# Kernel tuning notes

Hardware: AMD Instinct MI355X
Metric: run time of the kernel (lower is better)

Reference implementation:

```python
import jax, jax.numpy as jnp
import numpy as np

B, T, D, H, F = 2, 128, 256, 8, 64
C = H * F          # channels = 512
TEMB = 512         # time_embed_dim


def setup_inputs() -> dict:
    key = jax.random.key(0)
    ks = jax.random.split(key, 9)
    qk = jax.random.normal(ks[0], (B, D, H, T, F), jnp.float32)
    # integer-valued relative distances in [-(T-1), T-1], stored as float
    pairwise_distances = jax.random.randint(ks[1], (B, T, T), -(T - 1), T).astype(jnp.float32)
    temb = jax.random.normal(ks[2], (B, T, TEMB), jnp.float32)
    # linear layer params (note: original zero-inits w_out/b_out; we use random
    # values so the kernel correctness test is non-trivial)
    w_dist = jax.random.normal(ks[3], (C, 3), jnp.float32) / np.sqrt(3.0)
    b_dist = jax.random.normal(ks[4], (C,), jnp.float32) * 0.02
    w_time = jax.random.normal(ks[5], (C, TEMB), jnp.float32) / np.sqrt(TEMB)
    b_time = jax.random.normal(ks[6], (C,), jnp.float32) * 0.02
    w_out = jax.random.normal(ks[7], (C, C), jnp.float32) / np.sqrt(C)
    b_out = jax.random.normal(ks[8], (C,), jnp.float32) * 0.02
    return {"qk": qk, "pairwise_distances": pairwise_distances, "temb": temb,
            "w_dist": w_dist, "b_dist": b_dist, "w_time": w_time, "b_time": b_time,
            "w_out": w_out, "b_out": b_out}


def _rpe_net(pd, temb, w_dist, b_dist, w_time, b_time, w_out, b_out):
    # distance features: [B,T,T,3]
    dist_embs = jnp.stack([
        jnp.log1p(jnp.maximum(pd, 0.0)),
        jnp.log1p(jnp.maximum(-pd, 0.0)),
        (pd == 0).astype(pd.dtype),
    ], axis=-1)
    # [B,T,1,C] + [B,T,T,C]
    temb_emb = jnp.einsum('btk,ck->btc', temb, w_time) + b_time
    emb = temb_emb[:, :, None, :] + jnp.einsum('btsk,ck->btsc', dist_embs, w_dist) + b_dist
    r = jnp.einsum('btsc,oc->btso', jax.nn.silu(emb), w_out) + b_out
    return r.reshape(B, T, T, H, F)  # [B,T,S,H,F]


def reference(qk, pairwise_distances, temb, w_dist, b_dist, w_time, b_time, w_out, b_out):
    R = _rpe_net(pairwise_distances, temb, w_dist, b_dist, w_time, b_time, w_out, b_out)
    # mode == 'qk'
    return jnp.einsum('bdhtf,btshf->bdhts', qk, R)
```

## Files before the change

### kernel.cpp

```cpp
#include <hip/hip_runtime.h>
#include <hip/hip_bf16.h>
#include <math.h>

typedef __attribute__((ext_vector_type(8))) short short8;
typedef __attribute__((ext_vector_type(4))) float f32x4;

#define B_    2
#define T_    128
#define D_    256
#define H_    8
#define F_    64
#define C_    512
#define TEMB_ 512

static __device__ __forceinline__ unsigned short f2bf(float f) {
  __hip_bfloat16 h = __float2bfloat16(f);
  return reinterpret_cast<unsigned short&>(h);
}
static __device__ __forceinline__ unsigned int pk2(float a, float b) {
  return (unsigned int)f2bf(a) | ((unsigned int)f2bf(b) << 16);
}

__global__ __launch_bounds__(256) void k_pre(
    const float* __restrict__ temb, const float* __restrict__ w_time,
    const float* __restrict__ b_time, const float* __restrict__ b_dist,
    const float* __restrict__ w_out, const float* __restrict__ w_dist,
    float* __restrict__ base, short* __restrict__ wsw, float* __restrict__ wdT)
{
  const int tid = threadIdx.x;
  if (blockIdx.x >= 64) {
    int gid = (blockIdx.x - 64) * 256 + tid;
    for (int s = gid; s < 32768; s += 16384) {
      int oi = s >> 10, rem = s & 1023, kjg = rem >> 6, l = rem & 63;
      int o = oi * 16 + (l & 15), c = kjg * 32 + (l >> 4) * 8;
      const float* src = w_out + (size_t)o * C_ + c;
      float4 a = *reinterpret_cast<const float4*>(src);
      float4 b = *reinterpret_cast<const float4*>(src + 4);
      uint4 v; v.x = pk2(a.x, a.y); v.y = pk2(a.z, a.w);
      v.z = pk2(b.x, b.y); v.w = pk2(b.z, b.w);
      *reinterpret_cast<uint4*>(wsw + (size_t)s * 8) = v;
    }
    if (gid < C_) {
      wdT[0 * C_ + gid] = w_dist[gid * 3 + 0];
      wdT[1 * C_ + gid] = w_dist[gid * 3 + 1];
      wdT[2 * C_ + gid] = w_dist[gid * 3 + 2];
    }
    return;
  }
  __shared__ float tt[32][64];
  __shared__ float wt[64][65];
  const int bt0 = (blockIdx.x & 7) * 32;
  const int c0  = (blockIdx.x >> 3) * 64;
  const int cl  = tid & 63;
  const int g   = tid >> 6;
  float acc[8] = {0.f,0.f,0.f,0.f,0.f,0.f,0.f,0.f};

  for (int k0 = 0; k0 < TEMB_; k0 += 64) {
#pragma unroll
    for (int i = 0; i < 8; ++i) {
      int idx = tid + i * 256; int r = idx >> 6, k = idx & 63;
      tt[r][k] = temb[(size_t)(bt0 + r) * TEMB_ + k0 + k];
    }
#pragma unroll
    for (int i = 0; i < 16; ++i) {
      int idx = tid + i * 256; int r = idx >> 6, k = idx & 63;
      wt[r][k] = w_time[(size_t)(c0 + r) * TEMB_ + k0 + k];
    }
    __syncthreads();
#pragma unroll
    for (int k = 0; k < 64; ++k) {
      float w = wt[cl][k];
#pragma unroll
      for (int j = 0; j < 8; ++j) acc[j] += tt[g + 4 * j][k] * w;
    }
    __syncthreads();
  }
  float bb = b_time[c0 + cl] + b_dist[c0 + cl];
#pragma unroll
  for (int j = 0; j < 8; ++j)
    base[(size_t)(bt0 + g + 4 * j) * C_ + c0 + cl] = acc[j] + bb;
}

__global__ __launch_bounds__(512, 4) void k_rpe(
    const float* __restrict__ pd, const float* __restrict__ base,
    const float* __restrict__ wdT, const short* __restrict__ wsw,
    const float* __restrict__ b_out, unsigned short* __restrict__ Rg)
{
  __shared__ __align__(16) short At[8192];
  __shared__ float df[3][T_];

  const int bx   = blockIdx.x;
  const int bt   = bx >> 1;
  const int half = bx & 1;
  const int b    = bt >> 7;
  const int t    = bt & 127;
  const int tid  = threadIdx.x;
  const int lane = tid & 63;
  const int wave = tid >> 6;
  const int lanem = lane & 15;
  const int laneg = lane >> 4;

  if (tid < T_) {
    float p = pd[((size_t)b * T_ + t) * T_ + tid];
    df[0][tid] = log1pf(fmaxf(p, 0.f));
    df[1][tid] = log1pf(fmaxf(-p, 0.f));
    df[2][tid] = (p == 0.f) ? 1.f : 0.f;
  }

  const int wm = wave >> 2;
  const int wn = wave & 3;
  const int s_low = tid & 15;
  const int cg    = (tid >> 4) & 7;
  const int si_b  = (tid >> 7) * 2;
  const int kjA   = cg >> 2;
  const int cgl   = cg & 3;
  const int laneslotA = s_low + 16 * cgl;
  const float* baserow = base + (size_t)bt * C_;

  f32x4 acc[4][4];
#pragma unroll
  for (int mi = 0; mi < 4; ++mi)
#pragma unroll
    for (int ni = 0; ni < 4; ++ni) acc[mi][ni] = (f32x4){0.f, 0.f, 0.f, 0.f};

  for (int kt = 0; kt < 8; ++kt) {
    __syncthreads();
    short8 b0[4], b1[4];
#pragma unroll
    for (int ni = 0; ni < 4; ++ni) {
      int oi = half * 16 + wn * 4 + ni;
      b0[ni] = *reinterpret_cast<const short8*>(
          wsw + ((size_t)(oi * 16 + kt * 2 + 0) * 64 + lane) * 8);
    }
    {
      const int cglob = kt * 64 + cg * 8;
      float4 bs0 = *reinterpret_cast<const float4*>(baserow + cglob);
      float4 bs1 = *reinterpret_cast<const float4*>(baserow + cglob + 4);
      float4 wa0 = *reinterpret_cast<const float4*>(wdT + cglob);
      float4 wa1 = *reinterpret_cast<const float4*>(wdT + cglob + 4);
      float4 wb0 = *reinterpret_cast<const float4*>(wdT + C_ + cglob);
      float4 wb1 = *reinterpret_cast<const float4*>(wdT + C_ + cglob + 4);
      float4 wc0 = *reinterpret_cast<const float4*>(wdT + 2 * C_ + cglob);
      float4 wc1 = *reinterpret_cast<const float4*>(wdT + 2 * C_ + cglob + 4);
#pragma unroll
      for (int q = 0; q < 2; ++q) {
        int si = si_b + q;
        int s  = si * 16 + s_low;
        float d0 = df[0][s], d1 = df[1][s], d2 = df[2][s];
        uint4 v;
        {
          float x0 = bs0.x + d0 * wa0.x + d1 * wb0.x + d2 * wc0.x;
          float x1 = bs0.y + d0 * wa0.y + d1 * wb0.y + d2 * wc0.y;
          float x2 = bs0.z + d0 * wa0.z + d1 * wb0.z + d2 * wc0.z;
          float x3 = bs0.w + d0 * wa0.w + d1 * wb0.w + d2 * wc0.w;
          x0 = x0 / (1.f + __expf(-x0)); x1 = x1 / (1.f + __expf(-x1));
          x2 = x2 / (1.f + __expf(-x2)); x3 = x3 / (1.f + __expf(-x3));
          v.x = pk2(x0, x1); v.y = pk2(x2, x3);
        }
        {
          float x0 = bs1.x + d0 * wa1.x + d1 * wb1.x + d2 * wc1.x;
          float x1 = bs1.y + d0 * wa1.y + d1 * wb1.y + d2 * wc1.y;
          float x2 = bs1.z + d0 * wa1.z + d1 * wb1.z + d2 * wc1.z;
          float x3 = bs1.w + d0 * wa1.w + d1 * wb1.w + d2 * wc1.w;
          x0 = x0 / (1.f + __expf(-x0)); x1 = x1 / (1.f + __expf(-x1));
          x2 = x2 / (1.f + __expf(-x2)); x3 = x3 / (1.f + __expf(-x3));
          v.z = pk2(x0, x1); v.w = pk2(x2, x3);
        }
        *reinterpret_cast<uint4*>(&At[((si * 2 + kjA) * 64 + laneslotA) * 8]) = v;
      }
    }
#pragma unroll
    for (int ni = 0; ni < 4; ++ni) {
      int oi = half * 16 + wn * 4 + ni;
      b1[ni] = *reinterpret_cast<const short8*>(
          wsw + ((size_t)(oi * 16 + kt * 2 + 1) * 64 + lane) * 8);
    }
    __syncthreads();
    {
      short8 a[4];
#pragma unroll
      for (int mi = 0; mi < 4; ++mi)
        a[mi] = *reinterpret_cast<const short8*>(
            &At[(((wm * 4 + mi) * 2 + 0) * 64 + lane) * 8]);
#pragma unroll
      for (int ni = 0; ni < 4; ++ni)
#pragma unroll
        for (int mi = 0; mi < 4; ++mi)
          acc[mi][ni] = __builtin_amdgcn_mfma_f32_16x16x32_bf16(
              b0[ni], a[mi], acc[mi][ni], 0, 0, 0);
#pragma unroll
      for (int mi = 0; mi < 4; ++mi)
        a[mi] = *reinterpret_cast<const short8*>(
            &At[(((wm * 4 + mi) * 2 + 1) * 64 + lane) * 8]);
#pragma unroll
      for (int ni = 0; ni < 4; ++ni)
#pragma unroll
        for (int mi = 0; mi < 4; ++mi)
          acc[mi][ni] = __builtin_amdgcn_mfma_f32_16x16x32_bf16(
              b1[ni], a[mi], acc[mi][ni], 0, 0, 0);
    }
  }

  unsigned short* Rbt = Rg + (size_t)bt * T_ * C_;
#pragma unroll
  for (int ni = 0; ni < 4; ++ni) {
    const int o0 = half * 256 + wn * 64 + ni * 16 + laneg * 4;
    const float4 bo4 = *reinterpret_cast<const float4*>(b_out + o0);
#pragma unroll
    for (int mi = 0; mi < 4; ++mi) {
      const int s = wm * 64 + mi * 16 + lanem;
      uint2 v;
      v.x = pk2(acc[mi][ni][0] + bo4.x, acc[mi][ni][1] + bo4.y);
      v.y = pk2(acc[mi][ni][2] + bo4.z, acc[mi][ni][3] + bo4.w);
      *reinterpret_cast<uint2*>(Rbt + (size_t)s * C_ + o0) = v;
    }
  }
}

__global__ __launch_bounds__(256, 4) void k_qkr(
    const float* __restrict__ qk, const unsigned short* __restrict__ Rg,
    float* __restrict__ out)
{
  __shared__ __align__(16) float stage[4][2048];

  const int bx = blockIdx.x;
  const int h  = bx & 7;
  const int bt = bx >> 3;
  const int b  = bt >> 7;
  const int t  = bt & 127;
  const int tid  = threadIdx.x;
  const int lane = tid & 63;
  const int wave = tid >> 6;
  const int lanem = lane & 15;
  const int laneg = lane >> 4;
  const int d0w = wave * 64;

  const size_t HTF = (size_t)H_ * T_ * F_;
  const size_t HTT = (size_t)H_ * T_ * T_;
  const float* qkb = qk + (size_t)b * D_ * HTF + (size_t)h * T_ * F_ + (size_t)t * F_;
  float* outb = out + (size_t)b * D_ * HTT + (size_t)h * T_ * T_ + (size_t)t * T_;
  const unsigned short* Rb = Rg + (size_t)bt * T_ * C_ + h * F_;

  float4 buf[4];
  {
    const float* src = qkb + (size_t)(d0w + lanem) * HTF + laneg * 8;
    buf[0] = *reinterpret_cast<const float4*>(src);
    buf[1] = *reinterpret_cast<const float4*>(src + 4);
    buf[2] = *reinterpret_cast<const float4*>(src + 32);
    buf[3] = *reinterpret_cast<const float4*>(src + 36);
  }

  short8 brf[2][8];
#pragma unroll
  for (int kj = 0; kj < 2; ++kj)
#pragma unroll
    for (int ni = 0; ni < 8; ++ni)
      brf[kj][ni] = *reinterpret_cast<const short8*>(
          Rb + (size_t)(ni * 16 + lanem) * C_ + kj * 32 + laneg * 8);

  char* stO = (char*)stage[wave];
  const int xw = lanem << 4;
  const int l5 = lane >> 5;
  const int sb = (lane & 31) * 16;

  for (int cc = 0; cc < 4; ++cc) {
    const int dbase = d0w + cc * 16;
    short8 qb0, qb1;
    {
      union { uint4 u; short8 s; } cv;
      cv.u.x = pk2(buf[0].x, buf[0].y); cv.u.y = pk2(buf[0].z, buf[0].w);
      cv.u.z = pk2(buf[1].x, buf[1].y); cv.u.w = pk2(buf[1].z, buf[1].w);
      qb0 = cv.s;
      cv.u.x = pk2(buf[2].x, buf[2].y); cv.u.y = pk2(buf[2].z, buf[2].w);
      cv.u.z = pk2(buf[3].x, buf[3].y); cv.u.w = pk2(buf[3].z, buf[3].w);
      qb1 = cv.s;
    }
    if (cc < 3) {
      const float* src = qkb + (size_t)(dbase + 16 + lanem) * HTF + laneg * 8;
      buf[0] = *reinterpret_cast<const float4*>(src);
      buf[1] = *reinterpret_cast<const float4*>(src + 4);
      buf[2] = *reinterpret_cast<const float4*>(src + 32);
      buf[3] = *reinterpret_cast<const float4*>(src + 36);
    }
    f32x4 ac[8];
#pragma unroll
    for (int ni = 0; ni < 8; ++ni) ac[ni] = (f32x4){0.f, 0.f, 0.f, 0.f};
#pragma unroll
    for (int ni = 0; ni < 8; ++ni)
      ac[ni] = __builtin_amdgcn_mfma_f32_16x16x32_bf16(brf[0][ni], qb0, ac[ni], 0, 0, 0);
#pragma unroll
    for (int ni = 0; ni < 8; ++ni)
      ac[ni] = __builtin_amdgcn_mfma_f32_16x16x32_bf16(brf[1][ni], qb1, ac[ni], 0, 0, 0);
#pragma unroll
    for (int ni = 0; ni < 8; ++ni)
      *reinterpret_cast<f32x4*>(
          stO + lanem * 512 + ((ni * 64 + laneg * 16) ^ xw)) = ac[ni];
#pragma unroll
    for (int i = 0; i < 8; ++i) {
      int r = i * 2 + l5;
      float4 v = *reinterpret_cast<const float4*>(
          stO + r * 512 + (sb ^ (r << 4)));
      *reinterpret_cast<float4*>(
          outb + (size_t)(dbase + r) * HTT + (lane & 31) * 4) = v;
    }
  }
}

extern "C" void kernel_launch(void* const* d_in, const int* in_sizes, int n_in,
                              void* d_out, int out_size, void* d_ws, size_t ws_size,
                              hipStream_t stream) {
  const float* qk     = (const float*)d_in[0];
  const float* pd     = (const float*)d_in[1];
  const float* temb   = (const float*)d_in[2];
  const float* w_dist = (const float*)d_in[3];
  const float* b_dist = (const float*)d_in[4];
  const float* w_time = (const float*)d_in[5];
  const float* b_time = (const float*)d_in[6];
  const float* w_out  = (const float*)d_in[7];
  const float* b_out  = (const float*)d_in[8];
  float* out = (float*)d_out;

  char* ws = (char*)d_ws;
  float* base          = (float*)(ws);
  float* wdT           = (float*)(ws + 524288);
  short* wsw           = (short*)(ws + 532480);
  unsigned short* Rg   = (unsigned short*)(ws + 1056768);

  hipLaunchKernelGGL(k_pre, dim3(128), dim3(256), 0, stream,
                     temb, w_time, b_time, b_dist, w_out, w_dist,
                     base, wsw, wdT);
  hipLaunchKernelGGL(k_rpe, dim3(2 * B_ * T_), dim3(512), 0, stream,
                     pd, base, wdT, wsw, b_out, Rg);
  hipLaunchKernelGGL(k_qkr, dim3(B_ * T_ * H_), dim3(256), 0, stream,
                     qk, Rg, out);
}
```

Baseline: 203.1 us.

## Remap qk·R kernel grid over d-groups and t-quarters, drop LDS staging

Each k_qkr block now covers a group of 16 d values and a quarter of t for a single (b,h), where before it covered one (b,t,h) across all d. Each wave loops over 8 t values, reloading the R tile and qk rows for every t. Because each t maps to a contiguous output row, the LDS transpose stage is removed and results are written straight to global memory as float4. The cost is that R is re-read from global or L2 by every d-group (16x reuse across blocks instead of within a block), and the output stores become 64-byte pieces per row rather than 512-byte coalesced rows.

```diff
diff --git a/kernel.cpp b/kernel.cpp
--- a/kernel.cpp
+++ b/kernel.cpp
@@ -221,88 +221,69 @@
     const float* __restrict__ qk, const unsigned short* __restrict__ Rg,
     float* __restrict__ out)
 {
-  __shared__ __align__(16) float stage[4][2048];
-
   const int bx = blockIdx.x;
-  const int h  = bx & 7;
-  const int bt = bx >> 3;
-  const int b  = bt >> 7;
-  const int t  = bt & 127;
+  const int g  = bx & 63;
+  const int dg = bx >> 6;
+  const int b  = g >> 5;
+  const int h  = (g >> 2) & 7;
+  const int tq = g & 3;
   const int tid  = threadIdx.x;
   const int lane = tid & 63;
   const int wave = tid >> 6;
   const int lanem = lane & 15;
   const int laneg = lane >> 4;
-  const int d0w = wave * 64;
 
   const size_t HTF = (size_t)H_ * T_ * F_;
   const size_t HTT = (size_t)H_ * T_ * T_;
-  const float* qkb = qk + (size_t)b * D_ * HTF + (size_t)h * T_ * F_ + (size_t)t * F_;
-  float* outb = out + (size_t)b * D_ * HTT + (size_t)h * T_ * T_ + (size_t)t * T_;
-  const unsigned short* Rb = Rg + (size_t)bt * T_ * C_ + h * F_;
-
-  float4 buf[4];
-  {
-    const float* src = qkb + (size_t)(d0w + lanem) * HTF + laneg * 8;
-    buf[0] = *reinterpret_cast<const float4*>(src);
-    buf[1] = *reinterpret_cast<const float4*>(src + 4);
-    buf[2] = *reinterpret_cast<const float4*>(src + 32);
-    buf[3] = *reinterpret_cast<const float4*>(src + 36);
-  }
-
-  short8 brf[2][8];
-#pragma unroll
-  for (int kj = 0; kj < 2; ++kj)
-#pragma unroll
-    for (int ni = 0; ni < 8; ++ni)
-      brf[kj][ni] = *reinterpret_cast<const short8*>(
-          Rb + (size_t)(ni * 16 + lanem) * C_ + kj * 32 + laneg * 8);
-
-  char* stO = (char*)stage[wave];
-  const int xw = lanem << 4;
-  const int l5 = lane >> 5;
-  const int sb = (lane & 31) * 16;
-
-  for (int cc = 0; cc < 4; ++cc) {
-    const int dbase = d0w + cc * 16;
+  const int d = dg * 16 + lanem;
+
+  const float* qkrow = qk + (size_t)b * D_ * HTF + (size_t)d * HTF
+                          + (size_t)h * T_ * F_ + laneg * 8;
+  float* outrow = out + (size_t)(b * D_ + d) * HTT + (size_t)h * T_ * T_;
+  const unsigned short* Rbase = Rg + (size_t)b * T_ * T_ * C_
+                                   + (size_t)lanem * C_ + h * F_ + laneg * 8;
+
+  const int t0 = tq * 32 + wave * 8;
+#pragma unroll
+  for (int ti = 0; ti < 8; ++ti) {
+    const int t = t0 + ti;
+    const float* qs = qkrow + (size_t)t * F_;
+    float4 q0 = *reinterpret_cast<const float4*>(qs);
+    float4 q1 = *reinterpret_cast<const float4*>(qs + 4);
+    float4 q2 = *reinterpret_cast<const float4*>(qs + 32);
+    float4 q3 = *reinterpret_cast<const float4*>(qs + 36);
+    const unsigned short* rs = Rbase + (size_t)t * T_ * C_;
+    short8 av[2][8];
+#pragma unroll
+    for (int kj = 0; kj < 2; ++kj)
+#pragma unroll
+      for (int ni = 0; ni < 8; ++ni)
+        av[kj][ni] = *reinterpret_cast<const short8*>(
+            rs + (size_t)ni * 16 * C_ + kj * 32);
     short8 qb0, qb1;
     {
       union { uint4 u; short8 s; } cv;
-      cv.u.x = pk2(buf[0].x, buf[0].y); cv.u.y = pk2(buf[0].z, buf[0].w);
-      cv.u.z = pk2(buf[1].x, buf[1].y); cv.u.w = pk2(buf[1].z, buf[1].w);
+      cv.u.x = pk2(q0.x, q0.y); cv.u.y = pk2(q0.z, q0.w);
+      cv.u.z = pk2(q1.x, q1.y); cv.u.w = pk2(q1.z, q1.w);
       qb0 = cv.s;
-      cv.u.x = pk2(buf[2].x, buf[2].y); cv.u.y = pk2(buf[2].z, buf[2].w);
-      cv.u.z = pk2(buf[3].x, buf[3].y); cv.u.w = pk2(buf[3].z, buf[3].w);
+      cv.u.x = pk2(q2.x, q2.y); cv.u.y = pk2(q2.z, q2.w);
+      cv.u.z = pk2(q3.x, q3.y); cv.u.w = pk2(q3.z, q3.w);
       qb1 = cv.s;
     }
-    if (cc < 3) {
-      const float* src = qkb + (size_t)(dbase + 16 + lanem) * HTF + laneg * 8;
-      buf[0] = *reinterpret_cast<const float4*>(src);
-      buf[1] = *reinterpret_cast<const float4*>(src + 4);
-      buf[2] = *reinterpret_cast<const float4*>(src + 32);
-      buf[3] = *reinterpret_cast<const float4*>(src + 36);
-    }
     f32x4 ac[8];
 #pragma unroll
     for (int ni = 0; ni < 8; ++ni) ac[ni] = (f32x4){0.f, 0.f, 0.f, 0.f};
 #pragma unroll
     for (int ni = 0; ni < 8; ++ni)
-      ac[ni] = __builtin_amdgcn_mfma_f32_16x16x32_bf16(brf[0][ni], qb0, ac[ni], 0, 0, 0);
+      ac[ni] = __builtin_amdgcn_mfma_f32_16x16x32_bf16(av[0][ni], qb0, ac[ni], 0, 0, 0);
 #pragma unroll
     for (int ni = 0; ni < 8; ++ni)
-      ac[ni] = __builtin_amdgcn_mfma_f32_16x16x32_bf16(brf[1][ni], qb1, ac[ni], 0, 0, 0);
+      ac[ni] = __builtin_amdgcn_mfma_f32_16x16x32_bf16(av[1][ni], qb1, ac[ni], 0, 0, 0);
+    float* os = outrow + (size_t)t * T_ + laneg * 4;
 #pragma unroll
     for (int ni = 0; ni < 8; ++ni)
-      *reinterpret_cast<f32x4*>(
-          stO + lanem * 512 + ((ni * 64 + laneg * 16) ^ xw)) = ac[ni];
-#pragma unroll
-    for (int i = 0; i < 8; ++i) {
-      int r = i * 2 + l5;
-      float4 v = *reinterpret_cast<const float4*>(
-          stO + r * 512 + (sb ^ (r << 4)));
-      *reinterpret_cast<float4*>(
-          outb + (size_t)(dbase + r) * HTT + (lane & 31) * 4) = v;
-    }
+      *reinterpret_cast<float4*>(os + ni * 16) =
+          (float4){ac[ni][0], ac[ni][1], ac[ni][2], ac[ni][3]};
   }
 }
 
@@ -331,6 +312,6 @@
                      base, wsw, wdT);
   hipLaunchKernelGGL(k_rpe, dim3(2 * B_ * T_), dim3(512), 0, stream,
                      pd, base, wdT, wsw, b_out, Rg);
-  hipLaunchKernelGGL(k_qkr, dim3(B_ * T_ * H_), dim3(256), 0, stream,
+  hipLaunchKernelGGL(k_qkr, dim3(1024), dim3(256), 0, stream,
                      qk, Rg, out);
 }
```

New measurement: 281.1 us. 1.38x slower.

## Stage qk tiles via async global-to-LDS DMA and store outputs directly

Applied to the files above, without the earlier changes.

Replaces register prefetch of qk rows with global_load_lds DMA into double-buffered, XOR-swizzled per-wave LDS buffers, using explicit vmcnt waits to overlap loads with MFMA work. The output transpose through LDS is dropped, and MFMA results are written straight to global as float4 per lane. This is meant to cut register pressure and LDS round-trips, but the direct stores use 16-byte segments scattered across rows, so they are less coalesced. The hand-counted vmcnt values are fragile if the compiler reorders memory operations.

```diff
diff --git a/kernel.cpp b/kernel.cpp
--- a/kernel.cpp
+++ b/kernel.cpp
@@ -12,6 +12,8 @@
 #define F_    64
 #define C_    512
 #define TEMB_ 512
+#define HTF_  65536
+#define HTT_  131072
 
 static __device__ __forceinline__ unsigned short f2bf(float f) {
   __hip_bfloat16 h = __float2bfloat16(f);
@@ -19,6 +21,12 @@
 }
 static __device__ __forceinline__ unsigned int pk2(float a, float b) {
   return (unsigned int)f2bf(a) | ((unsigned int)f2bf(b) << 16);
+}
+
+static __device__ __forceinline__ void dma16(const float* g, float* l) {
+  __builtin_amdgcn_global_load_lds(
+      (const __attribute__((address_space(1))) unsigned int*)g,
+      (__attribute__((address_space(3))) unsigned int*)l, 16, 0, 0);
 }
 
 __global__ __launch_bounds__(256) void k_pre(
@@ -221,7 +229,7 @@
     const float* __restrict__ qk, const unsigned short* __restrict__ Rg,
     float* __restrict__ out)
 {
-  __shared__ __align__(16) float stage[4][2048];
+  __shared__ __align__(16) float st[4][2][1024];
 
   const int bx = blockIdx.x;
   const int h  = bx & 7;
@@ -233,22 +241,10 @@
   const int wave = tid >> 6;
   const int lanem = lane & 15;
   const int laneg = lane >> 4;
-  const int d0w = wave * 64;
-
-  const size_t HTF = (size_t)H_ * T_ * F_;
-  const size_t HTT = (size_t)H_ * T_ * T_;
-  const float* qkb = qk + (size_t)b * D_ * HTF + (size_t)h * T_ * F_ + (size_t)t * F_;
-  float* outb = out + (size_t)b * D_ * HTT + (size_t)h * T_ * T_ + (size_t)t * T_;
+
+  const float* qkb = qk + (size_t)b * D_ * HTF_ + (size_t)h * T_ * F_ + (size_t)t * F_;
+  float* outb = out + (size_t)b * D_ * HTT_ + (size_t)h * T_ * T_ + (size_t)t * T_;
   const unsigned short* Rb = Rg + (size_t)bt * T_ * C_ + h * F_;
-
-  float4 buf[4];
-  {
-    const float* src = qkb + (size_t)(d0w + lanem) * HTF + laneg * 8;
-    buf[0] = *reinterpret_cast<const float4*>(src);
-    buf[1] = *reinterpret_cast<const float4*>(src + 4);
-    buf[2] = *reinterpret_cast<const float4*>(src + 32);
-    buf[3] = *reinterpret_cast<const float4*>(src + 36);
-  }
 
   short8 brf[2][8];
 #pragma unroll
@@ -258,29 +254,54 @@
       brf[kj][ni] = *reinterpret_cast<const short8*>(
           Rb + (size_t)(ni * 16 + lanem) * C_ + kj * 32 + laneg * 8);
 
-  char* stO = (char*)stage[wave];
-  const int xw = lanem << 4;
-  const int l5 = lane >> 5;
-  const int sb = (lane & 31) * 16;
-
-  for (int cc = 0; cc < 4; ++cc) {
-    const int dbase = d0w + cc * 16;
+  float* buf0 = &st[wave][0][0];
+  float* buf1 = &st[wave][1][0];
+  auto STAGE = [&](float* buf, int c) {
+#pragma unroll
+    for (int j = 0; j < 4; ++j) {
+      const int dl = j * 4 + laneg;
+      const int g  = lanem ^ ((dl & 7) << 1);
+      const float* src = qkb + (size_t)(c * 16 + dl) * HTF_ + g * 4;
+      dma16(src, buf + j * 256);
+    }
+  };
+
+  const int c0 = wave * 4;
+  STAGE(buf0, c0 + 0);
+  STAGE(buf1, c0 + 1);
+  __builtin_amdgcn_sched_barrier(0);
+
+#pragma unroll
+  for (int i = 0; i < 4; ++i) {
+    const int c = c0 + i;
+    float* cur = (i & 1) ? buf1 : buf0;
+    if (i == 0)      asm volatile("s_waitcnt vmcnt(4)"  ::: "memory");
+    else if (i == 1) asm volatile("s_waitcnt vmcnt(12)" ::: "memory");
+    else if (i == 2) asm volatile("s_waitcnt vmcnt(20)" ::: "memory");
+    else             asm volatile("s_waitcnt vmcnt(16)" ::: "memory");
+    __builtin_amdgcn_sched_barrier(0);
+
+    const int key = (lanem & 7) << 1;
+    const int bd  = lanem * 64;
+    const int g0  = (2 * laneg) ^ key;
+    const int g1  = (8 + 2 * laneg) ^ key;
+    float4 f0 = *reinterpret_cast<const float4*>(cur + bd + g0 * 4);
+    float4 f1 = *reinterpret_cast<const float4*>(cur + bd + g0 * 4 + 4);
+    float4 f2 = *reinterpret_cast<const float4*>(cur + bd + g1 * 4);
+    float4 f3 = *reinterpret_cast<const float4*>(cur + bd + g1 * 4 + 4);
+    asm volatile("s_waitcnt lgkmcnt(0)" ::: "memory");
+    __builtin_amdgcn_sched_barrier(0);
+    if (i < 2) STAGE(cur, c + 2);
+
     short8 qb0, qb1;
     {
       union { uint4 u; short8 s; } cv;
-      cv.u.x = pk2(buf[0].x, buf[0].y); cv.u.y = pk2(buf[0].z, buf[0].w);
-      cv.u.z = pk2(buf[1].x, buf[1].y); cv.u.w = pk2(buf[1].z, buf[1].w);
+      cv.u.x = pk2(f0.x, f0.y); cv.u.y = pk2(f0.z, f0.w);
+      cv.u.z = pk2(f1.x, f1.y); cv.u.w = pk2(f1.z, f1.w);
       qb0 = cv.s;
-      cv.u.x = pk2(buf[2].x, buf[2].y); cv.u.y = pk2(buf[2].z, buf[2].w);
-      cv.u.z = pk2(buf[3].x, buf[3].y); cv.u.w = pk2(buf[3].z, buf[3].w);
+      cv.u.x = pk2(f2.x, f2.y); cv.u.y = pk2(f2.z, f2.w);
+      cv.u.z = pk2(f3.x, f3.y); cv.u.w = pk2(f3.z, f3.w);
       qb1 = cv.s;
-    }
-    if (cc < 3) {
-      const float* src = qkb + (size_t)(dbase + 16 + lanem) * HTF + laneg * 8;
-      buf[0] = *reinterpret_cast<const float4*>(src);
-      buf[1] = *reinterpret_cast<const float4*>(src + 4);
-      buf[2] = *reinterpret_cast<const float4*>(src + 32);
-      buf[3] = *reinterpret_cast<const float4*>(src + 36);
     }
     f32x4 ac[8];
 #pragma unroll
@@ -291,18 +312,12 @@
 #pragma unroll
     for (int ni = 0; ni < 8; ++ni)
       ac[ni] = __builtin_amdgcn_mfma_f32_16x16x32_bf16(brf[1][ni], qb1, ac[ni], 0, 0, 0);
+
+    float* od = outb + (size_t)(c * 16 + lanem) * HTT_ + laneg * 4;
 #pragma unroll
     for (int ni = 0; ni < 8; ++ni)
-      *reinterpret_cast<f32x4*>(
-          stO + lanem * 512 + ((ni * 64 + laneg * 16) ^ xw)) = ac[ni];
-#pragma unroll
-    for (int i = 0; i < 8; ++i) {
-      int r = i * 2 + l5;
-      float4 v = *reinterpret_cast<const float4*>(
-          stO + r * 512 + (sb ^ (r << 4)));
-      *reinterpret_cast<float4*>(
-          outb + (size_t)(dbase + r) * HTT + (lane & 31) * 4) = v;
-    }
+      *reinterpret_cast<float4*>(od + ni * 16) =
+          (float4){ac[ni][0], ac[ni][1], ac[ni][2], ac[ni][3]};
   }
 }
 
```

Measured after the change: 195.4 us. 1.04x faster.
